# Kernel tuning notes

Measured on AMD Instinct MI355X. Metric: run time of the kernel, lower is better.

## Reference

```python
import jax, jax.numpy as jnp
import numpy as np

B, S, HID = 1, 4096, 2048
H, KVH, D = 8, 4, 256
QR, KR, VR = 6, 2, 2
WINDOW = 1024
SOFTCAP = 50.0
SCALING = 256.0 ** -0.5  # query_pre_attn_scalar ** -0.5
EPS = 1e-6
NEG = -2.3819763e38


def _rope(x, cos, sin):
    # x: [B,S,R,D]; cos/sin: [S,D//2] -> rotate interleaved complex pairs
    xr = x.reshape(*x.shape[:-1], D // 2, 2)
    x1, x2 = xr[..., 0], xr[..., 1]
    c = cos[None, :, None, :]
    s = sin[None, :, None, :]
    out = jnp.stack([x1 * c - x2 * s, x1 * s + x2 * c], axis=-1)
    return out.reshape(x.shape)


def _rmsnorm(x, w):
    var = jnp.mean(x * x, axis=-1, keepdims=True)
    return x * jax.lax.rsqrt(var + EPS) * (1.0 + w)


def setup_inputs() -> dict:
    key = jax.random.key(0)
    ks = jax.random.split(key, 12)
    sc = HID ** -0.5
    pos = np.arange(S, dtype=np.float32)
    inv = 1.0 / (10000.0 ** (np.arange(0, D, 2, dtype=np.float32) / D))
    fr = pos[:, None] * inv[None, :]
    return {
        'hidden_states': jax.random.normal(ks[0], (B, S, HID), jnp.float32),
        'freqs_cos': jnp.asarray(np.cos(fr), jnp.float32),
        'freqs_sin': jnp.asarray(np.sin(fr), jnp.float32),
        'W_A_q': jax.random.normal(ks[1], (H * QR, HID), jnp.float32) * sc,
        'W_A_k': jax.random.normal(ks[2], (KVH * KR, HID), jnp.float32) * sc,
        'W_A_v': jax.random.normal(ks[3], (KVH * VR, HID), jnp.float32) * sc,
        'W_B_q': jax.random.normal(ks[4], (QR * D, HID), jnp.float32) * sc,
        'W_B_k': jax.random.normal(ks[5], (KR * D, HID), jnp.float32) * sc,
        'W_B_v': jax.random.normal(ks[6], (VR * D, HID), jnp.float32) * sc,
        'W_o': jax.random.normal(ks[7], (HID, H * D), jnp.float32) * (H * D) ** -0.5,
        'q_norm_w': jnp.zeros((D,), jnp.float32),
        'k_norm_w': jnp.zeros((D,), jnp.float32),
        'k_cache_A': jnp.zeros((B, S, KVH, KR), jnp.float32),
        'k_cache_B': jnp.zeros((B, S, KR, D), jnp.float32),
        'v_cache_A': jnp.zeros((B, S, KVH, VR), jnp.float32),
        'v_cache_B': jnp.zeros((B, S, VR, D), jnp.float32),
        'kv_write_indices': jnp.arange(S, dtype=jnp.int32),
    }


def reference(hidden_states, freqs_cos, freqs_sin, W_A_q, W_A_k, W_A_v,
              W_B_q, W_B_k, W_B_v, W_o, q_norm_w, k_norm_w,
              k_cache_A, k_cache_B, v_cache_A, v_cache_B, kv_write_indices):
    x = hidden_states  # [B,S,HID]
    # factorized projections
    A_q = (x @ W_A_q.T).reshape(B, S, H, QR)
    A_k = (x @ W_A_k.T).reshape(B, S, KVH, KR)
    A_v = (x @ W_A_v.T).reshape(B, S, KVH, VR)
    B_q = (x @ W_B_q.T).reshape(B, S, QR, D)
    B_k = (x @ W_B_k.T).reshape(B, S, KR, D)
    B_v = (x @ W_B_v.T).reshape(B, S, VR, D)
    # RoPE on head-dim factors of Q and K
    B_q = _rope(B_q, freqs_cos, freqs_sin)
    B_k = _rope(B_k, freqs_cos, freqs_sin)
    # write factors into the TPA KV cache
    k_cache_A = k_cache_A.at[:, kv_write_indices].set(A_k)
    k_cache_B = k_cache_B.at[:, kv_write_indices].set(B_k)
    v_cache_A = v_cache_A.at[:, kv_write_indices].set(A_v)
    v_cache_B = v_cache_B.at[:, kv_write_indices].set(B_v)
    # reconstruct Q/K/V from rank-R tensor products (mean over rank)
    q = jnp.einsum('bshr,bsrd->bshd', A_q, B_q) / QR          # [B,S,H,D]
    k = jnp.einsum('btkr,btrd->btkd', k_cache_A, k_cache_B) / KR  # [B,T,KVH,D]
    v = jnp.einsum('btkr,btrd->btkd', v_cache_A, v_cache_B) / VR
    # QK RMSNorm
    q = _rmsnorm(q, q_norm_w)
    k = _rmsnorm(k, k_norm_w)
    # GQA: expand KV heads to query heads
    rep = H // KVH
    k = jnp.repeat(k, rep, axis=2)  # [B,T,H,D]
    v = jnp.repeat(v, rep, axis=2)
    # scores with softcapping + sliding-window causal mask
    scores = jnp.einsum('bshd,bthd->bhst', q * SCALING, k)
    scores = jnp.tanh(scores / SOFTCAP) * SOFTCAP
    q_pos = kv_write_indices[:, None]        # [S,1]
    k_pos = jnp.arange(S, dtype=jnp.int32)[None, :]  # [1,T]
    diff = q_pos - k_pos
    allowed = (diff >= 0) & (diff < WINDOW)
    scores = jnp.where(allowed[None, None], scores, NEG)
    probs = jax.nn.softmax(scores, axis=-1)
    out = jnp.einsum('bhst,bthd->bshd', probs, v).reshape(B, S, H * D)
    return out @ W_o.T
```

## Files before the change

kernel.cpp:

```cpp
#include <hip/hip_runtime.h>
#include <hip/hip_bf16.h>
#include <cstdint>
#include <cstddef>

constexpr int SEQ   = 4096;
constexpr int HIDN  = 2048;
constexpr int NHEAD = 8;
constexpr int NKVH  = 4;
constexpr int DH    = 256;
constexpr int NPROJ = 2624;
constexpr int NPROJP= 2688;
constexpr int WIN   = 1024;

typedef __attribute__((ext_vector_type(4))) float f32x4;
typedef __attribute__((ext_vector_type(8))) short bf16x8;
typedef unsigned short u16;

__device__ __forceinline__ u16 f2bf(float x) {
  union { float f; uint32_t u; } v; v.f = x;
  uint32_t r = v.u + 0x7fffu + ((v.u >> 16) & 1u);
  return (u16)(r >> 16);
}
__device__ __forceinline__ float bf2f(u16 v) {
  union { uint32_t u; float f; } w; w.u = (uint32_t)v << 16; return w.f;
}

__device__ __forceinline__ uint32_t cvtpk(float lo, float hi) {
  uint32_t r;
  asm("v_cvt_pk_bf16_f32 %0, %1, %2" : "=v"(r) : "v"(lo), "v"(hi));
  return r;
}

__device__ __forceinline__ void gl_lds16(const u16* g, u16* l) {
  __builtin_amdgcn_global_load_lds(
      (const __attribute__((address_space(1))) uint32_t*)g,
      (__attribute__((address_space(3))) uint32_t*)l, 16, 0, 0);
}

__device__ __forceinline__ void sync_vm() {
  asm volatile("s_waitcnt vmcnt(0)" ::: "memory");
  __builtin_amdgcn_s_barrier();
  __builtin_amdgcn_sched_barrier(0);
}

__device__ __forceinline__ int xcd_swz(int wg, int nwg) {
  const int q = nwg >> 3, r = nwg & 7;
  const int xcd = wg & 7, lo = wg >> 3;
  return (xcd < r ? xcd * (q + 1) : r * (q + 1) + (xcd - r) * q) + lo;
}

__global__ __launch_bounds__(256) void k_cvt(const float* __restrict__ src,
                                             u16* __restrict__ dst, int n4) {
  int i = blockIdx.x * 256 + threadIdx.x;
  if (i >= n4) return;
  float4 v = ((const float4*)src)[i];
  ushort4 o; o.x = f2bf(v.x); o.y = f2bf(v.y); o.z = f2bf(v.z); o.w = f2bf(v.w);
  ((ushort4*)dst)[i] = o;
}

__global__ __launch_bounds__(256) void k_wcat(
    const float* __restrict__ waq, const float* __restrict__ wak,
    const float* __restrict__ wav, const float* __restrict__ wbq,
    const float* __restrict__ wbk, const float* __restrict__ wbv,
    u16* __restrict__ wcat) {
  const int r = blockIdx.x;
  const int col0 = threadIdx.x * 8;
  u16* out = wcat + (size_t)r * HIDN + col0;
  const float* src = nullptr; int rr = 0;
  if      (r < 48)   { src = waq; rr = r; }
  else if (r < 56)   { src = wak; rr = r - 48; }
  else if (r < 64)   { src = wav; rr = r - 56; }
  else if (r < 1600) { src = wbq; rr = r - 64; }
  else if (r < 2112) { src = wbk; rr = r - 1600; }
  else if (r < 2624) { src = wbv; rr = r - 2112; }
  if (!src) {
    ushort4 z = {0,0,0,0}; ((ushort4*)out)[0] = z; ((ushort4*)out)[1] = z; return;
  }
  const float* s = src + (size_t)rr * HIDN + col0;
#pragma unroll
  for (int i = 0; i < 2; ++i) {
    float4 v = ((const float4*)s)[i];
    ushort4 o; o.x = f2bf(v.x); o.y = f2bf(v.y); o.z = f2bf(v.z); o.w = f2bf(v.w);
    ((ushort4*)out)[i] = o;
  }
}

template<int OBF16>
__global__ __launch_bounds__(256)
void k_gemm_bt(const u16* __restrict__ A, const u16* __restrict__ Bm,
               void* __restrict__ Cv, int M, int N, int K) {
  __shared__ u16 lA[2][128 * 32];
  __shared__ u16 lB[2][128 * 32];
  const int tid = threadIdx.x;
  const int wid = tid >> 6, lane = tid & 63;
  const int l15 = lane & 15, g = lane >> 4;
  const int nwg = gridDim.x * gridDim.y;
  int wg = xcd_swz(blockIdx.y * gridDim.x + blockIdx.x, nwg);
  const int m0 = (wg / gridDim.x) * 128, n0 = (wg % gridDim.x) * 128;
  const int wr = wid >> 1, wc = wid & 1;
  f32x4 acc[4][4];
#pragma unroll
  for (int m = 0; m < 4; ++m)
#pragma unroll
    for (int n = 0; n < 4; ++n) acc[m][n] = (f32x4){0.f,0.f,0.f,0.f};
  const int NT = K >> 5;

  auto stage = [&](int buf, int kt) {
    const int k0 = kt << 5;
#pragma unroll
    for (int i = 0; i < 2; ++i) {
      const int u = i * 256 + tid;
      const int row = u >> 2, cs = u & 3;
      const int cc = cs ^ ((row >> 1) & 3);
      gl_lds16(A  + (size_t)(m0 + row) * K + k0 + cc * 8, &lA[buf][(i*256 + wid*64) * 8]);
      gl_lds16(Bm + (size_t)(n0 + row) * K + k0 + cc * 8, &lB[buf][(i*256 + wid*64) * 8]);
    }
  };

  stage(0, 0);
  int cur = 0;
  for (int kt = 0; kt < NT; ++kt) {
    __syncthreads();
    if (kt + 1 < NT) stage(cur ^ 1, kt + 1);
    bf16x8 af[4], bfr[4];
#pragma unroll
    for (int m = 0; m < 4; ++m) {
      const int row = wr*64 + m*16 + l15;
      const int cc = g ^ ((row >> 1) & 3);
      af[m] = *(const bf16x8*)&lA[cur][row*32 + cc*8];
    }
#pragma unroll
    for (int n = 0; n < 4; ++n) {
      const int row = wc*64 + n*16 + l15;
      const int cc = g ^ ((row >> 1) & 3);
      bfr[n] = *(const bf16x8*)&lB[cur][row*32 + cc*8];
    }
    __builtin_amdgcn_s_setprio(1);
#pragma unroll
    for (int m = 0; m < 4; ++m)
#pragma unroll
      for (int n = 0; n < 4; ++n)
        acc[m][n] = __builtin_amdgcn_mfma_f32_16x16x32_bf16(af[m], bfr[n], acc[m][n], 0, 0, 0);
    __builtin_amdgcn_s_setprio(0);
    cur ^= 1;
  }
#pragma unroll
  for (int m = 0; m < 4; ++m)
#pragma unroll
    for (int n = 0; n < 4; ++n)
#pragma unroll
      for (int j = 0; j < 4; ++j) {
        const int row = m0 + wr*64 + m*16 + g*4 + j;
        const int col = n0 + wc*64 + n*16 + l15;
        if constexpr (OBF16) ((u16*)Cv)[(size_t)row * N + col] = f2bf(acc[m][n][j]);
        else                 ((float*)Cv)[(size_t)row * N + col] = acc[m][n][j];
      }
}

__global__ __launch_bounds__(256)
void k_qkv(const u16* __restrict__ Y, const float* __restrict__ cosT,
           const float* __restrict__ sinT, const float* __restrict__ qw,
           const float* __restrict__ kw, u16* __restrict__ q_s,
           u16* __restrict__ k_s, u16* __restrict__ v_s) {
  const int s = blockIdx.x;
  const int d = threadIdx.x;
  __shared__ float row[NPROJ];
  __shared__ float red[12][4];
  const u16* yr = Y + (size_t)s * NPROJP;
  for (int u4 = d; u4 < NPROJ/4; u4 += 256) {
    ushort4 v4 = ((const ushort4*)yr)[u4];
    row[u4*4+0] = bf2f(v4.x); row[u4*4+1] = bf2f(v4.y);
    row[u4*4+2] = bf2f(v4.z); row[u4*4+3] = bf2f(v4.w);
  }
  __syncthreads();
  const int i = d >> 1;
  const float cf = cosT[s * 128 + i];
  const float sf = sinT[s * 128 + i];
  const bool odd = d & 1;
  float bq[6], bk[2], bv[2];
#pragma unroll
  for (int r = 0; r < 6; ++r) {
    float x1 = row[64 + r*256 + 2*i], x2 = row[64 + r*256 + 2*i + 1];
    bq[r] = odd ? (x1*sf + x2*cf) : (x1*cf - x2*sf);
  }
#pragma unroll
  for (int r = 0; r < 2; ++r) {
    float x1 = row[1600 + r*256 + 2*i], x2 = row[1600 + r*256 + 2*i + 1];
    bk[r] = odd ? (x1*sf + x2*cf) : (x1*cf - x2*sf);
    bv[r] = row[2112 + r*256 + d];
  }
  float qv[8], kv[4], vv[4];
#pragma unroll
  for (int h = 0; h < 8; ++h) {
    float a = 0.f;
#pragma unroll
    for (int r = 0; r < 6; ++r) a += row[h*6 + r] * bq[r];
    qv[h] = a * (1.0f / 6.0f);
  }
#pragma unroll
  for (int c = 0; c < 4; ++c) {
    kv[c] = (row[48 + c*2]*bk[0] + row[48 + c*2 + 1]*bk[1]) * 0.5f;
    vv[c] = (row[56 + c*2]*bv[0] + row[56 + c*2 + 1]*bv[1]) * 0.5f;
  }
  const int lane = d & 63, wv = d >> 6;
#pragma unroll
  for (int t = 0; t < 12; ++t) {
    float x = (t < 8) ? qv[t] : kv[t - 8];
    float ss = x * x;
#pragma unroll
    for (int off = 32; off > 0; off >>= 1) ss += __shfl_xor(ss, off);
    if (lane == 0) red[t][wv] = ss;
  }
  __syncthreads();
  const float qwf = 1.0f + qw[d], kwf = 1.0f + kw[d];
#pragma unroll
  for (int h = 0; h < 8; ++h) {
    float v = red[h][0] + red[h][1] + red[h][2] + red[h][3];
    float r = rsqrtf(v * (1.0f/256.0f) + 1e-6f);
    q_s[((size_t)s*8 + h)*256 + d] = f2bf(qv[h] * r * qwf * 0.0625f);
  }
#pragma unroll
  for (int c = 0; c < 4; ++c) {
    float v = red[8+c][0] + red[8+c][1] + red[8+c][2] + red[8+c][3];
    float r = rsqrtf(v * (1.0f/256.0f) + 1e-6f);
    k_s[((size_t)s*4 + c)*256 + d] = f2bf(kv[c] * r * kwf);
    v_s[((size_t)s*4 + c)*256 + d] = f2bf(vv[c]);
  }
}

__global__ __launch_bounds__(256)
void k_vt(const u16* __restrict__ v_s, u16* __restrict__ vT) {
  __shared__ u16 tile[64][72];
  const int s0 = blockIdx.x * 64, d0 = blockIdx.y * 64, c = blockIdx.z;
  const int tid = threadIdx.x;
#pragma unroll
  for (int it = 0; it < 2; ++it) {
    const int u = it * 256 + tid;
    const int r = u >> 3, cc = u & 7;
    const u16* s = &v_s[(((size_t)(s0 + r))*4 + c)*256 + d0 + cc*8];
    ushort4 a = *(const ushort4*)s, b = *(const ushort4*)(s + 4);
    tile[r][cc*8+0]=a.x; tile[r][cc*8+1]=a.y; tile[r][cc*8+2]=a.z; tile[r][cc*8+3]=a.w;
    tile[r][cc*8+4]=b.x; tile[r][cc*8+5]=b.y; tile[r][cc*8+6]=b.z; tile[r][cc*8+7]=b.w;
  }
  __syncthreads();
#pragma unroll
  for (int it = 0; it < 2; ++it) {
    const int u = it * 256 + tid;
    const int dr = u >> 3, sc = u & 7;
    ushort4 a, b;
    a.x = tile[sc*8+0][dr]; a.y = tile[sc*8+1][dr]; a.z = tile[sc*8+2][dr]; a.w = tile[sc*8+3][dr];
    b.x = tile[sc*8+4][dr]; b.y = tile[sc*8+5][dr]; b.z = tile[sc*8+6][dr]; b.w = tile[sc*8+7][dr];
    u16* o = vT + ((size_t)c*256 + d0 + dr)*SEQ + s0 + sc*8;
    *(ushort4*)o = a; *(ushort4*)(o + 4) = b;
  }
}

__global__ __launch_bounds__(256)
void k_attn(const u16* __restrict__ q_s, const u16* __restrict__ k_s,
            const u16* __restrict__ vT, const int* __restrict__ idx,
            u16* __restrict__ ao) {
  __shared__ u16 Kt[2][32 * 256];
  __shared__ u16 Vt[2][256 * 32];
  __shared__ u16 Pb[4][16 * 40];
  const int b = blockIdx.x;
  const int c = b & 3, qt = b >> 2;
  const int q0 = qt * 32;
  const int tid = threadIdx.x;
  const int wid = tid >> 6, lane = tid & 63;
  const int l15 = lane & 15, g = lane >> 4;
  const int h = 2*c + (wid >> 1);
  const int qsub = wid & 1;
  const int qrow = q0 + qsub*16 + l15;
  const int qpos = idx[qrow];

  bf16x8 qf[8];
  const u16* qb = q_s + ((size_t)qrow * 8 + h) * 256;
#pragma unroll
  for (int kk = 0; kk < 8; ++kk) qf[kk] = *(const bf16x8*)(qb + kk*32 + g*8);

  int kbase[8];
#pragma unroll
  for (int kk = 0; kk < 8; ++kk)
    kbase[kk] = l15*256 + (((4*kk + g) ^ (l15 & 7)) * 8);
  const int vbase = l15*32 + ((g ^ ((l15 >> 1) & 3)) * 8);
  u16* KtF = &Kt[0][0];
  u16* VtF = &Vt[0][0];
  u16* Pw  = &Pb[wid][0];

  f32x4 accO[16];
#pragma unroll
  for (int n = 0; n < 16; ++n) accO[n] = (f32x4){0.f,0.f,0.f,0.f};
  float mrun = -50.0f, lrun = 0.0f;

  int t0 = q0 - (WIN - 1); if (t0 < 0) t0 = 0;
  const int kt_lo = t0 >> 5, kt_hi = qt;

  const int srow = tid >> 5;
  const int scl  = (tid & 31) ^ srow;
  const int vdr  = tid >> 2;
  const int vlc  = (tid & 3) ^ ((tid >> 3) & 3);
  const u16* kg = k_s + (size_t)(kt_lo*32 + srow) * 1024 + c*256 + scl*8;
  const u16* vg = vT  + (size_t)c*1048576 + (size_t)vdr*4096 + kt_lo*32 + vlc*8;

  auto stage = [&](int buf) {
#pragma unroll
    for (int i = 0; i < 4; ++i)
      gl_lds16(kg + i*8192,   &Kt[buf][(i*256 + wid*64) * 8]);
#pragma unroll
    for (int i = 0; i < 4; ++i)
      gl_lds16(vg + i*262144, &Vt[buf][(i*256 + wid*64) * 8]);
  };

  stage(0);
  int cur = 0;
  for (int kt = kt_lo; kt <= kt_hi; ++kt) {
    const int k0 = kt * 32;
    sync_vm();
    if (kt < kt_hi) { kg += 32768; vg += 32; stage(cur ^ 1); }

    const int kco = cur * 8192;
    f32x4 s0 = (f32x4){0.f,0.f,0.f,0.f}, s1 = (f32x4){0.f,0.f,0.f,0.f};
    __builtin_amdgcn_s_setprio(1);
#pragma unroll
    for (int kk = 0; kk < 8; ++kk) {
      bf16x8 kf0 = *(const bf16x8*)&KtF[kbase[kk] + kco];
      bf16x8 kf1 = *(const bf16x8*)&KtF[kbase[kk] + kco + 4096];
      s0 = __builtin_amdgcn_mfma_f32_16x16x32_bf16(kf0, qf[kk], s0, 0, 0, 0);
      s1 = __builtin_amdgcn_mfma_f32_16x16x32_bf16(kf1, qf[kk], s1, 0, 0, 0);
    }
    __builtin_amdgcn_s_setprio(0);

    float tv[8];
#pragma unroll
    for (int nk = 0; nk < 2; ++nk)
#pragma unroll
      for (int j = 0; j < 4; ++j) {
        float x = (nk == 0) ? s0[j] : s1[j];
        float u = __builtin_amdgcn_exp2f(x * 0.05770780163555854f);
        tv[nk*4+j] = fmaf(-100.0f, __builtin_amdgcn_rcpf(1.0f + u), 50.0f);
      }
    const int dbase = qpos - k0;
    if (kt == kt_hi) {
#pragma unroll
      for (int nk = 0; nk < 2; ++nk)
#pragma unroll
        for (int j = 0; j < 4; ++j)
          if (nk*16 + g*4 + j > dbase) tv[nk*4+j] = -1e38f;
    } else if (k0 < q0 - 992) {
#pragma unroll
      for (int nk = 0; nk < 2; ++nk)
#pragma unroll
        for (int j = 0; j < 4; ++j)
          if (dbase - (nk*16 + g*4 + j) > 1023) tv[nk*4+j] = -1e38f;
    }

    float tmax = tv[0];
#pragma unroll
    for (int t = 1; t < 8; ++t) tmax = fmaxf(tmax, tv[t]);
    if (__any(tmax > mrun + 8.0f)) {
      float tq = fmaxf(tmax, __shfl_xor(tmax, 16));
      tq = fmaxf(tq, __shfl_xor(tq, 32));
      const float mnew = fmaxf(mrun, tq);
      const float scale = __builtin_amdgcn_exp2f((mrun - mnew) * 1.442695041f);
      float scj[4];
#pragma unroll
      for (int j = 0; j < 4; ++j) scj[j] = __shfl(scale, g*4 + j);
#pragma unroll
      for (int n = 0; n < 16; ++n) {
        accO[n][0] *= scj[0]; accO[n][1] *= scj[1];
        accO[n][2] *= scj[2]; accO[n][3] *= scj[3];
      }
      lrun *= scale;
      mrun = mnew;
    }
    const float mr2 = mrun * 1.442695041f;
    float p[8];
#pragma unroll
    for (int t = 0; t < 8; ++t) {
      p[t] = __builtin_amdgcn_exp2f(fmaf(tv[t], 1.442695041f, -mr2));
      lrun += p[t];
    }

    uint32_t a0 = cvtpk(p[0], p[1]), a1 = cvtpk(p[2], p[3]);
    uint32_t b0 = cvtpk(p[4], p[5]), b1 = cvtpk(p[6], p[7]);
    { uint2 w = {a0, a1}; *(uint2*)&Pw[l15*40 + g*4]      = w; }
    { uint2 w = {b0, b1}; *(uint2*)&Pw[l15*40 + 16 + g*4] = w; }
    bf16x8 pa = *(const bf16x8*)&Pw[l15*40 + g*8];
    const int vco = cur * 8192;
    __builtin_amdgcn_s_setprio(1);
#pragma unroll
    for (int n = 0; n < 16; ++n) {
      bf16x8 vf = *(const bf16x8*)&VtF[vbase + vco + n*512];
      accO[n] = __builtin_amdgcn_mfma_f32_16x16x32_bf16(pa, vf, accO[n], 0, 0, 0);
    }
    __builtin_amdgcn_s_setprio(0);
    cur ^= 1;
  }

  lrun += __shfl_xor(lrun, 16);
  lrun += __shfl_xor(lrun, 32);
  const float linv = __builtin_amdgcn_rcpf(lrun);
  float lj[4];
#pragma unroll
  for (int j = 0; j < 4; ++j) lj[j] = __shfl(linv, g*4 + j);
#pragma unroll
  for (int n = 0; n < 16; ++n)
#pragma unroll
    for (int j = 0; j < 4; ++j) {
      const int r = q0 + qsub*16 + g*4 + j;
      ao[(size_t)r * HIDN + h*256 + n*16 + l15] = f2bf(accO[n][j] * lj[j]);
    }
}

extern "C" void kernel_launch(void* const* d_in, const int* in_sizes, int n_in,
                              void* d_out, int out_size, void* d_ws, size_t ws_size,
                              hipStream_t stream) {
  const float* x    = (const float*)d_in[0];
  const float* fcos = (const float*)d_in[1];
  const float* fsin = (const float*)d_in[2];
  const float* waq  = (const float*)d_in[3];
  const float* wak  = (const float*)d_in[4];
  const float* wav  = (const float*)d_in[5];
  const float* wbq  = (const float*)d_in[6];
  const float* wbk  = (const float*)d_in[7];
  const float* wbv  = (const float*)d_in[8];
  const float* wo   = (const float*)d_in[9];
  const float* qnw  = (const float*)d_in[10];
  const float* knw  = (const float*)d_in[11];
  const int*   idx  = (const int*)d_in[16];
  float* out = (float*)d_out;

  char* p = (char*)d_ws;
  u16*  xb   = (u16*)p;                 p += (size_t)SEQ*HIDN*2;
  u16*  wcat = (u16*)p;                 p += (size_t)NPROJP*HIDN*2;
  u16*  wob  = (u16*)p;                 p += (size_t)HIDN*HIDN*2;
  u16*  ypr  = (u16*)p;                 p += (size_t)SEQ*NPROJP*2;
  u16*  q_s  = (u16*)p;                 p += (size_t)SEQ*NHEAD*DH*2;
  u16*  k_s  = (u16*)p;                 p += (size_t)SEQ*NKVH*DH*2;
  u16*  v_s  = (u16*)p;                 p += (size_t)SEQ*NKVH*DH*2;
  u16*  vT   = (u16*)p;                 p += (size_t)SEQ*NKVH*DH*2;
  u16*  ao   = (u16*)p;                 p += (size_t)SEQ*HIDN*2;

  k_cvt <<<(SEQ*HIDN/4 + 255)/256, 256, 0, stream>>>(x, xb, SEQ*HIDN/4);
  k_cvt <<<(HIDN*HIDN/4 + 255)/256, 256, 0, stream>>>(wo, wob, HIDN*HIDN/4);
  k_wcat<<<NPROJP, 256, 0, stream>>>(waq, wak, wav, wbq, wbk, wbv, wcat);
  k_gemm_bt<1><<<dim3(NPROJP/128, SEQ/128), 256, 0, stream>>>(xb, wcat, ypr, SEQ, NPROJP, HIDN);
  k_qkv <<<SEQ, 256, 0, stream>>>(ypr, fcos, fsin, qnw, knw, q_s, k_s, v_s);
  k_vt  <<<dim3(SEQ/64, DH/64, NKVH), 256, 0, stream>>>(v_s, vT);
  k_attn<<<dim3(SEQ/32 * NKVH), 256, 0, stream>>>(q_s, k_s, vT, idx, ao);
  k_gemm_bt<0><<<dim3(HIDN/128, SEQ/128), 256, 0, stream>>>(ao, wob, out, SEQ, HIDN, HIDN);
}
```

Measured before the change: 224.7 us.

## Use 16-key tiles in attention, skip out-of-window tiles per wave, drop P LDS roundtrip

```diff
diff --git a/kernel.cpp b/kernel.cpp
--- a/kernel.cpp
+++ b/kernel.cpp
@@ -14,6 +14,7 @@
 
 typedef __attribute__((ext_vector_type(4))) float f32x4;
 typedef __attribute__((ext_vector_type(8))) short bf16x8;
+typedef __attribute__((ext_vector_type(4))) short bf16x4;
 typedef unsigned short u16;
 
 __device__ __forceinline__ u16 f2bf(float x) {
@@ -255,13 +256,12 @@
   }
 }
 
-__global__ __launch_bounds__(256)
+__global__ __launch_bounds__(256, 4)
 void k_attn(const u16* __restrict__ q_s, const u16* __restrict__ k_s,
             const u16* __restrict__ vT, const int* __restrict__ idx,
             u16* __restrict__ ao) {
-  __shared__ u16 Kt[2][32 * 256];
-  __shared__ u16 Vt[2][256 * 32];
-  __shared__ u16 Pb[4][16 * 40];
+  __shared__ u16 Kt[2][16 * 256];
+  __shared__ u16 Vt[2][256 * 16];
   const int b = blockIdx.x;
   const int c = b & 3, qt = b >> 2;
   const int q0 = qt * 32;
@@ -278,14 +278,11 @@
 #pragma unroll
   for (int kk = 0; kk < 8; ++kk) qf[kk] = *(const bf16x8*)(qb + kk*32 + g*8);
 
-  int kbase[8];
-#pragma unroll
-  for (int kk = 0; kk < 8; ++kk)
-    kbase[kk] = l15*256 + (((4*kk + g) ^ (l15 & 7)) * 8);
-  const int vbase = l15*32 + ((g ^ ((l15 >> 1) & 3)) * 8);
+  const int sw = l15 & 7;
+  const int kread0 = l15 * 256;
+  const int vread0 = l15 * 16 + g * 4;
   u16* KtF = &Kt[0][0];
   u16* VtF = &Vt[0][0];
-  u16* Pw  = &Pb[wid][0];
 
   f32x4 accO[16];
 #pragma unroll
@@ -293,107 +290,92 @@
   float mrun = -50.0f, lrun = 0.0f;
 
   int t0 = q0 - (WIN - 1); if (t0 < 0) t0 = 0;
-  const int kt_lo = t0 >> 5, kt_hi = qt;
-
-  const int srow = tid >> 5;
-  const int scl  = (tid & 31) ^ srow;
-  const int vdr  = tid >> 2;
-  const int vlc  = (tid & 3) ^ ((tid >> 3) & 3);
-  const u16* kg = k_s + (size_t)(kt_lo*32 + srow) * 1024 + c*256 + scl*8;
-  const u16* vg = vT  + (size_t)c*1048576 + (size_t)vdr*4096 + kt_lo*32 + vlc*8;
+  const int kt_lo = t0 >> 4, kt_hi = 2*qt + 1;
+  const int whi = q0 + qsub*16 + 15;
+  const int wlo = whi - 1053;
+
+  const u16* kgp = k_s + (size_t)(kt_lo*16 + (tid>>5)) * 1024 + c*256
+                   + ((tid & 31) ^ ((tid >> 5) & 7)) * 8;
+  const u16* vgp = vT + (size_t)c*1048576 + (size_t)(tid>>1)*4096
+                   + kt_lo*16 + (tid & 1)*8;
 
   auto stage = [&](int buf) {
-#pragma unroll
-    for (int i = 0; i < 4; ++i)
-      gl_lds16(kg + i*8192,   &Kt[buf][(i*256 + wid*64) * 8]);
-#pragma unroll
-    for (int i = 0; i < 4; ++i)
-      gl_lds16(vg + i*262144, &Vt[buf][(i*256 + wid*64) * 8]);
+    gl_lds16(kgp,          &Kt[buf][(wid*64)*8]);
+    gl_lds16(kgp + 8192,   &Kt[buf][(256 + wid*64)*8]);
+    gl_lds16(vgp,          &Vt[buf][(wid*64)*8]);
+    gl_lds16(vgp + 524288, &Vt[buf][(256 + wid*64)*8]);
   };
 
   stage(0);
   int cur = 0;
   for (int kt = kt_lo; kt <= kt_hi; ++kt) {
-    const int k0 = kt * 32;
+    const int k0 = kt << 4;
     sync_vm();
-    if (kt < kt_hi) { kg += 32768; vg += 32; stage(cur ^ 1); }
-
-    const int kco = cur * 8192;
-    f32x4 s0 = (f32x4){0.f,0.f,0.f,0.f}, s1 = (f32x4){0.f,0.f,0.f,0.f};
-    __builtin_amdgcn_s_setprio(1);
-#pragma unroll
-    for (int kk = 0; kk < 8; ++kk) {
-      bf16x8 kf0 = *(const bf16x8*)&KtF[kbase[kk] + kco];
-      bf16x8 kf1 = *(const bf16x8*)&KtF[kbase[kk] + kco + 4096];
-      s0 = __builtin_amdgcn_mfma_f32_16x16x32_bf16(kf0, qf[kk], s0, 0, 0, 0);
-      s1 = __builtin_amdgcn_mfma_f32_16x16x32_bf16(kf1, qf[kk], s1, 0, 0, 0);
+    if (kt < kt_hi) { kgp += 16384; vgp += 16; stage(cur ^ 1); }
+
+    if (k0 >= wlo && k0 <= whi) {
+      const int kof = cur * 4096;
+      f32x4 s0 = (f32x4){0.f,0.f,0.f,0.f};
+      __builtin_amdgcn_s_setprio(1);
+#pragma unroll
+      for (int kk = 0; kk < 8; ++kk) {
+        bf16x8 kf = *(const bf16x8*)&KtF[kof + kread0 + ((((kk<<2)+g) ^ sw) << 3)];
+        s0 = __builtin_amdgcn_mfma_f32_16x16x32_bf16(kf, qf[kk], s0, 0, 0, 0);
+      }
+      __builtin_amdgcn_s_setprio(0);
+
+      float tv[4];
+#pragma unroll
+      for (int j = 0; j < 4; ++j) {
+        float u = __builtin_amdgcn_exp2f(s0[j] * 0.05770780163555854f);
+        tv[j] = fmaf(-100.0f, __builtin_amdgcn_rcpf(1.0f + u), 50.0f);
+      }
+      if (k0 == whi - 15) {
+#pragma unroll
+        for (int j = 0; j < 4; ++j)
+          if (k0 + g*4 + j > qpos) tv[j] = -1e38f;
+      } else if (k0 < whi - 1023) {
+#pragma unroll
+        for (int j = 0; j < 4; ++j)
+          if (qpos - (k0 + g*4 + j) > 1023) tv[j] = -1e38f;
+      }
+
+      float tmax = fmaxf(fmaxf(tv[0], tv[1]), fmaxf(tv[2], tv[3]));
+      if (__any(tmax > mrun + 8.0f)) {
+        float tq = fmaxf(tmax, __shfl_xor(tmax, 16));
+        tq = fmaxf(tq, __shfl_xor(tq, 32));
+        const float mnew = fmaxf(mrun, tq);
+        const float scale = __builtin_amdgcn_exp2f((mrun - mnew) * 1.442695041f);
+        float scj[4];
+#pragma unroll
+        for (int j = 0; j < 4; ++j) scj[j] = __shfl(scale, g*4 + j);
+#pragma unroll
+        for (int n = 0; n < 16; ++n) {
+          accO[n][0] *= scj[0]; accO[n][1] *= scj[1];
+          accO[n][2] *= scj[2]; accO[n][3] *= scj[3];
+        }
+        lrun *= scale;
+        mrun = mnew;
+      }
+      const float mr2 = mrun * 1.442695041f;
+      float p[4];
+#pragma unroll
+      for (int t = 0; t < 4; ++t) {
+        p[t] = __builtin_amdgcn_exp2f(fmaf(tv[t], 1.442695041f, -mr2));
+        lrun += p[t];
+      }
+
+      union { uint32_t u[2]; bf16x4 v; } pu;
+      pu.u[0] = cvtpk(p[0], p[1]); pu.u[1] = cvtpk(p[2], p[3]);
+      const int vof = cur * 4096;
+      __builtin_amdgcn_s_setprio(1);
+#pragma unroll
+      for (int n = 0; n < 16; ++n) {
+        bf16x4 vf = *(const bf16x4*)&VtF[vof + vread0 + n*256];
+        accO[n] = __builtin_amdgcn_mfma_f32_16x16x16bf16_1k(pu.v, vf, accO[n], 0, 0, 0);
+      }
+      __builtin_amdgcn_s_setprio(0);
     }
-    __builtin_amdgcn_s_setprio(0);
-
-    float tv[8];
-#pragma unroll
-    for (int nk = 0; nk < 2; ++nk)
-#pragma unroll
-      for (int j = 0; j < 4; ++j) {
-        float x = (nk == 0) ? s0[j] : s1[j];
-        float u = __builtin_amdgcn_exp2f(x * 0.05770780163555854f);
-        tv[nk*4+j] = fmaf(-100.0f, __builtin_amdgcn_rcpf(1.0f + u), 50.0f);
-      }
-    const int dbase = qpos - k0;
-    if (kt == kt_hi) {
-#pragma unroll
-      for (int nk = 0; nk < 2; ++nk)
-#pragma unroll
-        for (int j = 0; j < 4; ++j)
-          if (nk*16 + g*4 + j > dbase) tv[nk*4+j] = -1e38f;
-    } else if (k0 < q0 - 992) {
-#pragma unroll
-      for (int nk = 0; nk < 2; ++nk)
-#pragma unroll
-        for (int j = 0; j < 4; ++j)
-          if (dbase - (nk*16 + g*4 + j) > 1023) tv[nk*4+j] = -1e38f;
-    }
-
-    float tmax = tv[0];
-#pragma unroll
-    for (int t = 1; t < 8; ++t) tmax = fmaxf(tmax, tv[t]);
-    if (__any(tmax > mrun + 8.0f)) {
-      float tq = fmaxf(tmax, __shfl_xor(tmax, 16));
-      tq = fmaxf(tq, __shfl_xor(tq, 32));
-      const float mnew = fmaxf(mrun, tq);
-      const float scale = __builtin_amdgcn_exp2f((mrun - mnew) * 1.442695041f);
-      float scj[4];
-#pragma unroll
-      for (int j = 0; j < 4; ++j) scj[j] = __shfl(scale, g*4 + j);
-#pragma unroll
-      for (int n = 0; n < 16; ++n) {
-        accO[n][0] *= scj[0]; accO[n][1] *= scj[1];
-        accO[n][2] *= scj[2]; accO[n][3] *= scj[3];
-      }
-      lrun *= scale;
-      mrun = mnew;
-    }
-    const float mr2 = mrun * 1.442695041f;
-    float p[8];
-#pragma unroll
-    for (int t = 0; t < 8; ++t) {
-      p[t] = __builtin_amdgcn_exp2f(fmaf(tv[t], 1.442695041f, -mr2));
-      lrun += p[t];
-    }
-
-    uint32_t a0 = cvtpk(p[0], p[1]), a1 = cvtpk(p[2], p[3]);
-    uint32_t b0 = cvtpk(p[4], p[5]), b1 = cvtpk(p[6], p[7]);
-    { uint2 w = {a0, a1}; *(uint2*)&Pw[l15*40 + g*4]      = w; }
-    { uint2 w = {b0, b1}; *(uint2*)&Pw[l15*40 + 16 + g*4] = w; }
-    bf16x8 pa = *(const bf16x8*)&Pw[l15*40 + g*8];
-    const int vco = cur * 8192;
-    __builtin_amdgcn_s_setprio(1);
-#pragma unroll
-    for (int n = 0; n < 16; ++n) {
-      bf16x8 vf = *(const bf16x8*)&VtF[vbase + vco + n*512];
-      accO[n] = __builtin_amdgcn_mfma_f32_16x16x32_bf16(pa, vf, accO[n], 0, 0, 0);
-    }
-    __builtin_amdgcn_s_setprio(0);
     cur ^= 1;
   }
 
```

New measurement: 301.0 us. 1.34x slower.

## Enlarge attention tiles to 64 queries by 64 keys with 512-thread blocks

Applied to the files above, without the earlier changes.

```diff
diff --git a/kernel.cpp b/kernel.cpp
--- a/kernel.cpp
+++ b/kernel.cpp
@@ -255,21 +255,21 @@
   }
 }
 
-__global__ __launch_bounds__(256)
+__global__ __launch_bounds__(512, 2)
 void k_attn(const u16* __restrict__ q_s, const u16* __restrict__ k_s,
             const u16* __restrict__ vT, const int* __restrict__ idx,
             u16* __restrict__ ao) {
-  __shared__ u16 Kt[2][32 * 256];
-  __shared__ u16 Vt[2][256 * 32];
-  __shared__ u16 Pb[4][16 * 40];
+  __shared__ u16 Kt[2][64 * 256];
+  __shared__ u16 Vt[2][256 * 64];
+  __shared__ u16 Pb[8][16 * 68];
   const int b = blockIdx.x;
   const int c = b & 3, qt = b >> 2;
-  const int q0 = qt * 32;
+  const int q0 = qt * 64;
   const int tid = threadIdx.x;
   const int wid = tid >> 6, lane = tid & 63;
   const int l15 = lane & 15, g = lane >> 4;
-  const int h = 2*c + (wid >> 1);
-  const int qsub = wid & 1;
+  const int h = 2*c + (wid >> 2);
+  const int qsub = wid & 3;
   const int qrow = q0 + qsub*16 + l15;
   const int qpos = idx[qrow];
 
@@ -278,11 +278,11 @@
 #pragma unroll
   for (int kk = 0; kk < 8; ++kk) qf[kk] = *(const bf16x8*)(qb + kk*32 + g*8);
 
+  const int sw = l15 & 7;
   int kbase[8];
 #pragma unroll
   for (int kk = 0; kk < 8; ++kk)
-    kbase[kk] = l15*256 + (((4*kk + g) ^ (l15 & 7)) * 8);
-  const int vbase = l15*32 + ((g ^ ((l15 >> 1) & 3)) * 8);
+    kbase[kk] = l15*256 + ((((kk<<2)+g) ^ sw) << 3);
   u16* KtF = &Kt[0][0];
   u16* VtF = &Vt[0][0];
   u16* Pw  = &Pb[wid][0];
@@ -293,70 +293,68 @@
   float mrun = -50.0f, lrun = 0.0f;
 
   int t0 = q0 - (WIN - 1); if (t0 < 0) t0 = 0;
-  const int kt_lo = t0 >> 5, kt_hi = qt;
-
-  const int srow = tid >> 5;
-  const int scl  = (tid & 31) ^ srow;
-  const int vdr  = tid >> 2;
-  const int vlc  = (tid & 3) ^ ((tid >> 3) & 3);
-  const u16* kg = k_s + (size_t)(kt_lo*32 + srow) * 1024 + c*256 + scl*8;
-  const u16* vg = vT  + (size_t)c*1048576 + (size_t)vdr*4096 + kt_lo*32 + vlc*8;
+  const int kt_lo = t0 >> 6, kt_hi = qt;
+
+  const u16* kgp = k_s + (size_t)(kt_lo*64 + (tid>>5)) * 1024 + c*256
+                   + (((tid & 31) ^ ((tid >> 5) & 7)) << 3);
+  const u16* vgp = vT + (size_t)c*1048576 + (size_t)(tid>>3)*4096 + kt_lo*64
+                   + (((tid & 7) ^ ((tid >> 3) & 7)) << 3);
 
   auto stage = [&](int buf) {
 #pragma unroll
     for (int i = 0; i < 4; ++i)
-      gl_lds16(kg + i*8192,   &Kt[buf][(i*256 + wid*64) * 8]);
+      gl_lds16(kgp + i*16384,  &Kt[buf][(i*512 + wid*64) * 8]);
 #pragma unroll
     for (int i = 0; i < 4; ++i)
-      gl_lds16(vg + i*262144, &Vt[buf][(i*256 + wid*64) * 8]);
+      gl_lds16(vgp + i*262144, &Vt[buf][(i*512 + wid*64) * 8]);
   };
 
   stage(0);
   int cur = 0;
   for (int kt = kt_lo; kt <= kt_hi; ++kt) {
-    const int k0 = kt * 32;
+    const int k0 = kt << 6;
     sync_vm();
-    if (kt < kt_hi) { kg += 32768; vg += 32; stage(cur ^ 1); }
-
-    const int kco = cur * 8192;
-    f32x4 s0 = (f32x4){0.f,0.f,0.f,0.f}, s1 = (f32x4){0.f,0.f,0.f,0.f};
+    if (kt < kt_hi) { kgp += 65536; vgp += 64; stage(cur ^ 1); }
+
+    const int kco = cur * 16384;
+    f32x4 sc[4];
+#pragma unroll
+    for (int nk = 0; nk < 4; ++nk) sc[nk] = (f32x4){0.f,0.f,0.f,0.f};
     __builtin_amdgcn_s_setprio(1);
 #pragma unroll
-    for (int kk = 0; kk < 8; ++kk) {
-      bf16x8 kf0 = *(const bf16x8*)&KtF[kbase[kk] + kco];
-      bf16x8 kf1 = *(const bf16x8*)&KtF[kbase[kk] + kco + 4096];
-      s0 = __builtin_amdgcn_mfma_f32_16x16x32_bf16(kf0, qf[kk], s0, 0, 0, 0);
-      s1 = __builtin_amdgcn_mfma_f32_16x16x32_bf16(kf1, qf[kk], s1, 0, 0, 0);
-    }
+    for (int nk = 0; nk < 4; ++nk)
+#pragma unroll
+      for (int kk = 0; kk < 8; ++kk) {
+        bf16x8 kf = *(const bf16x8*)&KtF[kco + nk*4096 + kbase[kk]];
+        sc[nk] = __builtin_amdgcn_mfma_f32_16x16x32_bf16(kf, qf[kk], sc[nk], 0, 0, 0);
+      }
     __builtin_amdgcn_s_setprio(0);
 
-    float tv[8];
-#pragma unroll
-    for (int nk = 0; nk < 2; ++nk)
+    float tv[16];
+#pragma unroll
+    for (int nk = 0; nk < 4; ++nk)
 #pragma unroll
       for (int j = 0; j < 4; ++j) {
-        float x = (nk == 0) ? s0[j] : s1[j];
-        float u = __builtin_amdgcn_exp2f(x * 0.05770780163555854f);
+        float u = __builtin_amdgcn_exp2f(sc[nk][j] * 0.05770780163555854f);
         tv[nk*4+j] = fmaf(-100.0f, __builtin_amdgcn_rcpf(1.0f + u), 50.0f);
       }
-    const int dbase = qpos - k0;
     if (kt == kt_hi) {
 #pragma unroll
-      for (int nk = 0; nk < 2; ++nk)
+      for (int nk = 0; nk < 4; ++nk)
 #pragma unroll
         for (int j = 0; j < 4; ++j)
-          if (nk*16 + g*4 + j > dbase) tv[nk*4+j] = -1e38f;
-    } else if (k0 < q0 - 992) {
-#pragma unroll
-      for (int nk = 0; nk < 2; ++nk)
+          if (k0 + nk*16 + g*4 + j > qpos) tv[nk*4+j] = -1e38f;
+    } else if (kt == kt_lo) {
+#pragma unroll
+      for (int nk = 0; nk < 4; ++nk)
 #pragma unroll
         for (int j = 0; j < 4; ++j)
-          if (dbase - (nk*16 + g*4 + j) > 1023) tv[nk*4+j] = -1e38f;
+          if (qpos - (k0 + nk*16 + g*4 + j) > 1023) tv[nk*4+j] = -1e38f;
     }
 
     float tmax = tv[0];
 #pragma unroll
-    for (int t = 1; t < 8; ++t) tmax = fmaxf(tmax, tv[t]);
+    for (int t = 1; t < 16; ++t) tmax = fmaxf(tmax, tv[t]);
     if (__any(tmax > mrun + 8.0f)) {
       float tq = fmaxf(tmax, __shfl_xor(tmax, 16));
       tq = fmaxf(tq, __shfl_xor(tq, 32));
@@ -374,24 +372,29 @@
       mrun = mnew;
     }
     const float mr2 = mrun * 1.442695041f;
-    float p[8];
-#pragma unroll
-    for (int t = 0; t < 8; ++t) {
+    float p[16];
+#pragma unroll
+    for (int t = 0; t < 16; ++t) {
       p[t] = __builtin_amdgcn_exp2f(fmaf(tv[t], 1.442695041f, -mr2));
       lrun += p[t];
     }
 
-    uint32_t a0 = cvtpk(p[0], p[1]), a1 = cvtpk(p[2], p[3]);
-    uint32_t b0 = cvtpk(p[4], p[5]), b1 = cvtpk(p[6], p[7]);
-    { uint2 w = {a0, a1}; *(uint2*)&Pw[l15*40 + g*4]      = w; }
-    { uint2 w = {b0, b1}; *(uint2*)&Pw[l15*40 + 16 + g*4] = w; }
-    bf16x8 pa = *(const bf16x8*)&Pw[l15*40 + g*8];
-    const int vco = cur * 8192;
+#pragma unroll
+    for (int nk = 0; nk < 4; ++nk) {
+      uint2 w = { cvtpk(p[nk*4+0], p[nk*4+1]), cvtpk(p[nk*4+2], p[nk*4+3]) };
+      *(uint2*)&Pw[l15*68 + nk*16 + g*4] = w;
+    }
+    const int vco = cur * 16384;
     __builtin_amdgcn_s_setprio(1);
 #pragma unroll
-    for (int n = 0; n < 16; ++n) {
-      bf16x8 vf = *(const bf16x8*)&VtF[vbase + vco + n*512];
-      accO[n] = __builtin_amdgcn_mfma_f32_16x16x32_bf16(pa, vf, accO[n], 0, 0, 0);
+    for (int half = 0; half < 2; ++half) {
+      bf16x8 pa = *(const bf16x8*)&Pw[l15*68 + half*32 + g*8];
+#pragma unroll
+      for (int n = 0; n < 16; ++n) {
+        bf16x8 vf = *(const bf16x8*)&VtF[vco + (n*16 + l15)*64
+                                         + ((((half<<2)+g) ^ sw) << 3)];
+        accO[n] = __builtin_amdgcn_mfma_f32_16x16x32_bf16(pa, vf, accO[n], 0, 0, 0);
+      }
     }
     __builtin_amdgcn_s_setprio(0);
     cur ^= 1;
@@ -447,6 +450,6 @@
   k_gemm_bt<1><<<dim3(NPROJP/128, SEQ/128), 256, 0, stream>>>(xb, wcat, ypr, SEQ, NPROJP, HIDN);
   k_qkv <<<SEQ, 256, 0, stream>>>(ypr, fcos, fsin, qnw, knw, q_s, k_s, v_s);
   k_vt  <<<dim3(SEQ/64, DH/64, NKVH), 256, 0, stream>>>(v_s, vT);
-  k_attn<<<dim3(SEQ/32 * NKVH), 256, 0, stream>>>(q_s, k_s, vT, idx, ao);
+  k_attn<<<dim3(SEQ/64 * NKVH), 512, 0, stream>>>(q_s, k_s, vT, idx, ao);
   k_gemm_bt<0><<<dim3(HIDN/128, SEQ/128), 256, 0, stream>>>(ao, wob, out, SEQ, HIDN, HIDN);
 }
```

Result: faster. 217.9 us (-3.0%).

## Split attention KV range across two blocks and merge partials in a new kernel

Applied to the files above, without the earlier changes.

```diff
diff --git a/kernel.cpp b/kernel.cpp
--- a/kernel.cpp
+++ b/kernel.cpp
@@ -14,6 +14,7 @@
 
 typedef __attribute__((ext_vector_type(4))) float f32x4;
 typedef __attribute__((ext_vector_type(8))) short bf16x8;
+typedef __attribute__((ext_vector_type(4))) short bf16x4;
 typedef unsigned short u16;
 
 __device__ __forceinline__ u16 f2bf(float x) {
@@ -255,21 +256,20 @@
   }
 }
 
-__global__ __launch_bounds__(256)
+__global__ __launch_bounds__(512, 4)
 void k_attn(const u16* __restrict__ q_s, const u16* __restrict__ k_s,
             const u16* __restrict__ vT, const int* __restrict__ idx,
-            u16* __restrict__ ao) {
+            u16* __restrict__ op, float2* __restrict__ ml) {
   __shared__ u16 Kt[2][32 * 256];
   __shared__ u16 Vt[2][256 * 32];
-  __shared__ u16 Pb[4][16 * 40];
   const int b = blockIdx.x;
-  const int c = b & 3, qt = b >> 2;
-  const int q0 = qt * 32;
+  const int c = b & 3, sp = (b >> 2) & 1, qt = b >> 3;
+  const int q0 = qt * 64;
   const int tid = threadIdx.x;
   const int wid = tid >> 6, lane = tid & 63;
   const int l15 = lane & 15, g = lane >> 4;
-  const int h = 2*c + (wid >> 1);
-  const int qsub = wid & 1;
+  const int h = 2*c + (wid >> 2);
+  const int qsub = wid & 3;
   const int qrow = q0 + qsub*16 + l15;
   const int qpos = idx[qrow];
 
@@ -278,14 +278,13 @@
 #pragma unroll
   for (int kk = 0; kk < 8; ++kk) qf[kk] = *(const bf16x8*)(qb + kk*32 + g*8);
 
+  const int sw = l15 & 7;
   int kbase[8];
 #pragma unroll
   for (int kk = 0; kk < 8; ++kk)
-    kbase[kk] = l15*256 + (((4*kk + g) ^ (l15 & 7)) * 8);
-  const int vbase = l15*32 + ((g ^ ((l15 >> 1) & 3)) * 8);
+    kbase[kk] = l15*256 + ((((kk<<2)+g) ^ sw) << 3);
   u16* KtF = &Kt[0][0];
   u16* VtF = &Vt[0][0];
-  u16* Pw  = &Pb[wid][0];
 
   f32x4 accO[16];
 #pragma unroll
@@ -293,123 +292,155 @@
   float mrun = -50.0f, lrun = 0.0f;
 
   int t0 = q0 - (WIN - 1); if (t0 < 0) t0 = 0;
-  const int kt_lo = t0 >> 5, kt_hi = qt;
-
-  const int srow = tid >> 5;
-  const int scl  = (tid & 31) ^ srow;
-  const int vdr  = tid >> 2;
-  const int vlc  = (tid & 3) ^ ((tid >> 3) & 3);
-  const u16* kg = k_s + (size_t)(kt_lo*32 + srow) * 1024 + c*256 + scl*8;
-  const u16* vg = vT  + (size_t)c*1048576 + (size_t)vdr*4096 + kt_lo*32 + vlc*8;
+  const int klo_g = t0 >> 5, khi_g = (q0 + 63) >> 5;
+  const int nAll = khi_g - klo_g + 1, nHalf = nAll >> 1;
+  const int kt_lo = sp ? klo_g + nHalf : klo_g;
+  const int kt_hi = sp ? khi_g : klo_g + nHalf - 1;
+
+  const int whi = q0 + qsub*16 + 15;
+  const int wlo = q0 + qsub*16 - (WIN - 1);
+
+  const u16* kgp = k_s + (size_t)(kt_lo*32 + (tid>>5)) * 1024 + c*256
+                   + (((tid & 31) ^ ((tid >> 5) & 7)) << 3);
+  const u16* vgp = vT + (size_t)c*1048576 + (size_t)(tid>>2)*4096 + kt_lo*32
+                   + (((tid & 3) ^ ((tid >> 2) & 3)) << 3);
 
   auto stage = [&](int buf) {
-#pragma unroll
-    for (int i = 0; i < 4; ++i)
-      gl_lds16(kg + i*8192,   &Kt[buf][(i*256 + wid*64) * 8]);
-#pragma unroll
-    for (int i = 0; i < 4; ++i)
-      gl_lds16(vg + i*262144, &Vt[buf][(i*256 + wid*64) * 8]);
+    gl_lds16(kgp,          &Kt[buf][(wid*64)*8]);
+    gl_lds16(kgp + 16384,  &Kt[buf][(512 + wid*64)*8]);
+    gl_lds16(vgp,          &Vt[buf][(wid*64)*8]);
+    gl_lds16(vgp + 524288, &Vt[buf][(512 + wid*64)*8]);
   };
 
   stage(0);
   int cur = 0;
   for (int kt = kt_lo; kt <= kt_hi; ++kt) {
-    const int k0 = kt * 32;
+    const int k0 = kt << 5;
     sync_vm();
-    if (kt < kt_hi) { kg += 32768; vg += 32; stage(cur ^ 1); }
-
-    const int kco = cur * 8192;
-    f32x4 s0 = (f32x4){0.f,0.f,0.f,0.f}, s1 = (f32x4){0.f,0.f,0.f,0.f};
-    __builtin_amdgcn_s_setprio(1);
-#pragma unroll
-    for (int kk = 0; kk < 8; ++kk) {
-      bf16x8 kf0 = *(const bf16x8*)&KtF[kbase[kk] + kco];
-      bf16x8 kf1 = *(const bf16x8*)&KtF[kbase[kk] + kco + 4096];
-      s0 = __builtin_amdgcn_mfma_f32_16x16x32_bf16(kf0, qf[kk], s0, 0, 0, 0);
-      s1 = __builtin_amdgcn_mfma_f32_16x16x32_bf16(kf1, qf[kk], s1, 0, 0, 0);
+    if (kt < kt_hi) { kgp += 32768; vgp += 32; stage(cur ^ 1); }
+
+    if (k0 <= whi && k0 + 31 >= wlo) {
+      const int kco = cur * 8192;
+      f32x4 s0 = (f32x4){0.f,0.f,0.f,0.f}, s1 = (f32x4){0.f,0.f,0.f,0.f};
+      __builtin_amdgcn_s_setprio(1);
+#pragma unroll
+      for (int kk = 0; kk < 8; ++kk) {
+        bf16x8 kf0 = *(const bf16x8*)&KtF[kco + kbase[kk]];
+        bf16x8 kf1 = *(const bf16x8*)&KtF[kco + 4096 + kbase[kk]];
+        s0 = __builtin_amdgcn_mfma_f32_16x16x32_bf16(kf0, qf[kk], s0, 0, 0, 0);
+        s1 = __builtin_amdgcn_mfma_f32_16x16x32_bf16(kf1, qf[kk], s1, 0, 0, 0);
+      }
+      __builtin_amdgcn_s_setprio(0);
+
+      float tv[8];
+#pragma unroll
+      for (int nk = 0; nk < 2; ++nk)
+#pragma unroll
+        for (int j = 0; j < 4; ++j) {
+          float x = (nk == 0) ? s0[j] : s1[j];
+          float u = __builtin_amdgcn_exp2f(x * 0.05770780163555854f);
+          tv[nk*4+j] = fmaf(-100.0f, __builtin_amdgcn_rcpf(1.0f + u), 50.0f);
+        }
+      if (k0 + 31 > q0 + qsub*16) {
+#pragma unroll
+        for (int nk = 0; nk < 2; ++nk)
+#pragma unroll
+          for (int j = 0; j < 4; ++j)
+            if (k0 + nk*16 + g*4 + j > qpos) tv[nk*4+j] = -1e38f;
+      }
+      if (k0 < whi - (WIN - 1)) {
+#pragma unroll
+        for (int nk = 0; nk < 2; ++nk)
+#pragma unroll
+          for (int j = 0; j < 4; ++j)
+            if (qpos - (k0 + nk*16 + g*4 + j) > WIN - 1) tv[nk*4+j] = -1e38f;
+      }
+
+      float tmax = tv[0];
+#pragma unroll
+      for (int t = 1; t < 8; ++t) tmax = fmaxf(tmax, tv[t]);
+      if (__any(tmax > mrun + 8.0f)) {
+        float tq = fmaxf(tmax, __shfl_xor(tmax, 16));
+        tq = fmaxf(tq, __shfl_xor(tq, 32));
+        const float mnew = fmaxf(mrun, tq);
+        const float scale = __builtin_amdgcn_exp2f((mrun - mnew) * 1.442695041f);
+        float scj[4];
+#pragma unroll
+        for (int j = 0; j < 4; ++j) scj[j] = __shfl(scale, g*4 + j);
+#pragma unroll
+        for (int n = 0; n < 16; ++n) {
+          accO[n][0] *= scj[0]; accO[n][1] *= scj[1];
+          accO[n][2] *= scj[2]; accO[n][3] *= scj[3];
+        }
+        lrun *= scale;
+        mrun = mnew;
+      }
+      const float mr2 = mrun * 1.442695041f;
+      float p[8];
+#pragma unroll
+      for (int t = 0; t < 8; ++t) {
+        p[t] = __builtin_amdgcn_exp2f(fmaf(tv[t], 1.442695041f, -mr2));
+        lrun += p[t];
+      }
+
+      union { uint32_t u[2]; bf16x4 v; } pu0, pu1;
+      pu0.u[0] = cvtpk(p[0], p[1]); pu0.u[1] = cvtpk(p[2], p[3]);
+      pu1.u[0] = cvtpk(p[4], p[5]); pu1.u[1] = cvtpk(p[6], p[7]);
+      const int vco = cur * 8192;
+      const int part = g >> 1, off4 = (g & 1) * 4;
+      __builtin_amdgcn_s_setprio(1);
+#pragma unroll
+      for (int n = 0; n < 16; ++n) {
+        const int dr = n*16 + l15;
+        const int base = vco + dr*32 + off4;
+        bf16x4 vf0 = *(const bf16x4*)&VtF[base + ((part     ^ (dr & 3)) << 3)];
+        bf16x4 vf1 = *(const bf16x4*)&VtF[base + (((2+part) ^ (dr & 3)) << 3)];
+        accO[n] = __builtin_amdgcn_mfma_f32_16x16x16bf16_1k(pu0.v, vf0, accO[n], 0, 0, 0);
+        accO[n] = __builtin_amdgcn_mfma_f32_16x16x16bf16_1k(pu1.v, vf1, accO[n], 0, 0, 0);
+      }
+      __builtin_amdgcn_s_setprio(0);
     }
-    __builtin_amdgcn_s_setprio(0);
-
-    float tv[8];
-#pragma unroll
-    for (int nk = 0; nk < 2; ++nk)
-#pragma unroll
-      for (int j = 0; j < 4; ++j) {
-        float x = (nk == 0) ? s0[j] : s1[j];
-        float u = __builtin_amdgcn_exp2f(x * 0.05770780163555854f);
-        tv[nk*4+j] = fmaf(-100.0f, __builtin_amdgcn_rcpf(1.0f + u), 50.0f);
-      }
-    const int dbase = qpos - k0;
-    if (kt == kt_hi) {
-#pragma unroll
-      for (int nk = 0; nk < 2; ++nk)
-#pragma unroll
-        for (int j = 0; j < 4; ++j)
-          if (nk*16 + g*4 + j > dbase) tv[nk*4+j] = -1e38f;
-    } else if (k0 < q0 - 992) {
-#pragma unroll
-      for (int nk = 0; nk < 2; ++nk)
-#pragma unroll
-        for (int j = 0; j < 4; ++j)
-          if (dbase - (nk*16 + g*4 + j) > 1023) tv[nk*4+j] = -1e38f;
-    }
-
-    float tmax = tv[0];
-#pragma unroll
-    for (int t = 1; t < 8; ++t) tmax = fmaxf(tmax, tv[t]);
-    if (__any(tmax > mrun + 8.0f)) {
-      float tq = fmaxf(tmax, __shfl_xor(tmax, 16));
-      tq = fmaxf(tq, __shfl_xor(tq, 32));
-      const float mnew = fmaxf(mrun, tq);
-      const float scale = __builtin_amdgcn_exp2f((mrun - mnew) * 1.442695041f);
-      float scj[4];
-#pragma unroll
-      for (int j = 0; j < 4; ++j) scj[j] = __shfl(scale, g*4 + j);
-#pragma unroll
-      for (int n = 0; n < 16; ++n) {
-        accO[n][0] *= scj[0]; accO[n][1] *= scj[1];
-        accO[n][2] *= scj[2]; accO[n][3] *= scj[3];
-      }
-      lrun *= scale;
-      mrun = mnew;
-    }
-    const float mr2 = mrun * 1.442695041f;
-    float p[8];
-#pragma unroll
-    for (int t = 0; t < 8; ++t) {
-      p[t] = __builtin_amdgcn_exp2f(fmaf(tv[t], 1.442695041f, -mr2));
-      lrun += p[t];
-    }
-
-    uint32_t a0 = cvtpk(p[0], p[1]), a1 = cvtpk(p[2], p[3]);
-    uint32_t b0 = cvtpk(p[4], p[5]), b1 = cvtpk(p[6], p[7]);
-    { uint2 w = {a0, a1}; *(uint2*)&Pw[l15*40 + g*4]      = w; }
-    { uint2 w = {b0, b1}; *(uint2*)&Pw[l15*40 + 16 + g*4] = w; }
-    bf16x8 pa = *(const bf16x8*)&Pw[l15*40 + g*8];
-    const int vco = cur * 8192;
-    __builtin_amdgcn_s_setprio(1);
-#pragma unroll
-    for (int n = 0; n < 16; ++n) {
-      bf16x8 vf = *(const bf16x8*)&VtF[vbase + vco + n*512];
-      accO[n] = __builtin_amdgcn_mfma_f32_16x16x32_bf16(pa, vf, accO[n], 0, 0, 0);
-    }
-    __builtin_amdgcn_s_setprio(0);
     cur ^= 1;
   }
 
   lrun += __shfl_xor(lrun, 16);
   lrun += __shfl_xor(lrun, 32);
-  const float linv = __builtin_amdgcn_rcpf(lrun);
-  float lj[4];
-#pragma unroll
-  for (int j = 0; j < 4; ++j) lj[j] = __shfl(linv, g*4 + j);
+  if (g == 0) ml[(size_t)sp*SEQ*NHEAD + (size_t)qrow*NHEAD + h] = make_float2(mrun, lrun);
+  u16* opS = op + (size_t)sp*SEQ*HIDN;
 #pragma unroll
   for (int n = 0; n < 16; ++n)
 #pragma unroll
     for (int j = 0; j < 4; ++j) {
       const int r = q0 + qsub*16 + g*4 + j;
-      ao[(size_t)r * HIDN + h*256 + n*16 + l15] = f2bf(accO[n][j] * lj[j]);
+      opS[(size_t)r * HIDN + h*256 + n*16 + l15] = f2bf(accO[n][j]);
     }
+}
+
+__global__ __launch_bounds__(256)
+void k_mrg(const u16* __restrict__ op, const float2* __restrict__ ml,
+           u16* __restrict__ ao) {
+  const int q = blockIdx.x;
+  const int h = threadIdx.x >> 5;
+  const int dd = (threadIdx.x & 31) * 8;
+  const float2 a = ml[(size_t)q*NHEAD + h];
+  const float2 b = ml[(size_t)SEQ*NHEAD + (size_t)q*NHEAD + h];
+  const float M = fmaxf(a.x, b.x);
+  float w0 = __builtin_amdgcn_exp2f((a.x - M) * 1.442695041f);
+  float w1 = __builtin_amdgcn_exp2f((b.x - M) * 1.442695041f);
+  const float r = __builtin_amdgcn_rcpf(w0 * a.y + w1 * b.y);
+  w0 *= r; w1 *= r;
+  const size_t base = (size_t)q * HIDN + h*256 + dd;
+  bf16x8 o0 = *(const bf16x8*)&op[base];
+  bf16x8 o1 = *(const bf16x8*)&op[(size_t)SEQ*HIDN + base];
+  ushort4 lo, hi;
+  u16 ov[8];
+#pragma unroll
+  for (int j = 0; j < 8; ++j)
+    ov[j] = f2bf(w0 * bf2f((u16)o0[j]) + w1 * bf2f((u16)o1[j]));
+  lo.x = ov[0]; lo.y = ov[1]; lo.z = ov[2]; lo.w = ov[3];
+  hi.x = ov[4]; hi.y = ov[5]; hi.z = ov[6]; hi.w = ov[7];
+  *(ushort4*)&ao[base] = lo;
+  *(ushort4*)&ao[base + 4] = hi;
 }
 
 extern "C" void kernel_launch(void* const* d_in, const int* in_sizes, int n_in,
@@ -440,6 +471,8 @@
   u16*  v_s  = (u16*)p;                 p += (size_t)SEQ*NKVH*DH*2;
   u16*  vT   = (u16*)p;                 p += (size_t)SEQ*NKVH*DH*2;
   u16*  ao   = (u16*)p;                 p += (size_t)SEQ*HIDN*2;
+  u16*  op   = (u16*)p;                 p += (size_t)2*SEQ*HIDN*2;
+  float2* ml = (float2*)p;              p += (size_t)2*SEQ*NHEAD*sizeof(float2);
 
   k_cvt <<<(SEQ*HIDN/4 + 255)/256, 256, 0, stream>>>(x, xb, SEQ*HIDN/4);
   k_cvt <<<(HIDN*HIDN/4 + 255)/256, 256, 0, stream>>>(wo, wob, HIDN*HIDN/4);
@@ -447,6 +480,7 @@
   k_gemm_bt<1><<<dim3(NPROJP/128, SEQ/128), 256, 0, stream>>>(xb, wcat, ypr, SEQ, NPROJP, HIDN);
   k_qkv <<<SEQ, 256, 0, stream>>>(ypr, fcos, fsin, qnw, knw, q_s, k_s, v_s);
   k_vt  <<<dim3(SEQ/64, DH/64, NKVH), 256, 0, stream>>>(v_s, vT);
-  k_attn<<<dim3(SEQ/32 * NKVH), 256, 0, stream>>>(q_s, k_s, vT, idx, ao);
+  k_attn<<<dim3(SEQ/64 * 2 * NKVH), 512, 0, stream>>>(q_s, k_s, vT, idx, op, ml);
+  k_mrg <<<SEQ, 256, 0, stream>>>(op, ml, ao);
   k_gemm_bt<0><<<dim3(HIDN/128, SEQ/128), 256, 0, stream>>>(ao, wob, out, SEQ, HIDN, HIDN);
 }
```

New measurement: 295.4 us. +31.5%, slower.
